# Optimization experiments

Measured on AMD Instinct MI355X. Metric: run time of the kernel, lower is better.

Reference implementation:

```python
import jax, jax.numpy as jnp
import numpy as np

N_STEPS = 20      # max(n_steps_al, n_steps_kc)
ALPHA   = 0.9     # membrane decay exp(-dt/tau_m)
V_TH    = 1.0     # spiking threshold
G_SOMA  = 0.3     # dendrite->axon coupling conductance (2-compartment KC)
APL_GAIN = 1.0    # graded APL gain
I_SCALE = 0.5     # graded ORN drive scale
BETA    = 10.0    # surrogate-gradient sharpness ('soft' sigmoid)

@jax.custom_vjp
def spike(x):
    return (x > 0).astype(x.dtype)

def _spike_fwd(x):
    return spike(x), x

def _spike_bwd(x, g):
    s = jax.nn.sigmoid(BETA * x)
    return (g * BETA * s * (1.0 - s),)

spike.defvjp(_spike_fwd, _spike_bwd)


def _sparse_w(key, shape, density):
    k1, k2 = jax.random.split(key)
    mask = jax.random.bernoulli(k1, density, shape)
    w = jax.random.uniform(k2, shape)
    return (mask * w).astype(jnp.float32)


def setup_inputs() -> dict:
    key = jax.random.key(0)
    ks = jax.random.split(key, 10)
    batch, n_or, n_orn, n_ln, n_pn, n_kc, n_odors = 4096, 21, 42, 56, 42, 2000, 34
    or_input = jax.random.uniform(ks[0], (batch, n_or), dtype=jnp.float32)
    or_gains = jnp.ones((n_or,), jnp.float32)
    # fixed OR->ORN mapping: OR i drives left (2i) and right (2i+1) ORNs
    m = np.zeros((n_or, n_orn), np.float32)
    for i in range(n_or):
        m[i, 2 * i] = 1.0
        m[i, 2 * i + 1] = 1.0
    mapping = jnp.asarray(m)
    orn_to_pn = _sparse_w(ks[1], (n_orn, n_pn), 0.3)
    orn_to_ln = _sparse_w(ks[2], (n_orn, n_ln), 0.3)
    ln_to_pn = _sparse_w(ks[3], (n_ln, n_pn), 0.3)
    pn_to_kc = _sparse_w(ks[4], (n_pn, n_kc), 0.15)  # ~6 PN claws per KC
    kc_to_apl = jax.random.uniform(ks[5], (n_kc, 1), dtype=jnp.float32) * 0.01
    apl_to_kc = jax.random.uniform(ks[6], (1, n_kc), dtype=jnp.float32)
    dec_w = jax.random.normal(ks[7], (n_kc, n_odors), dtype=jnp.float32) * 0.02
    dec_b = jnp.zeros((n_odors,), jnp.float32)
    return {"or_input": or_input, "or_gains": or_gains, "mapping": mapping,
            "orn_to_pn": orn_to_pn, "orn_to_ln": orn_to_ln, "ln_to_pn": ln_to_pn,
            "pn_to_kc": pn_to_kc, "kc_to_apl": kc_to_apl, "apl_to_kc": apl_to_kc,
            "dec_w": dec_w, "dec_b": dec_b}


def reference(or_input, or_gains, mapping, orn_to_pn, orn_to_ln, ln_to_pn,
              pn_to_kc, kc_to_apl, apl_to_kc, dec_w, dec_b):
    B = or_input.shape[0]
    n_orn, n_pn = orn_to_pn.shape
    n_ln = orn_to_ln.shape[1]
    n_kc = pn_to_kc.shape[1]
    # OR transduction: graded, learnable per-OR gain
    orn_drive = (or_input * jax.nn.softplus(or_gains)) @ mapping  # [B, n_orn]

    z = lambda n: jnp.zeros((B, n), or_input.dtype)
    carry0 = (z(n_orn), z(n_ln), z(n_pn), z(n_kc), z(n_kc), z(1), z(n_kc))

    def step(carry, _):
        v_orn, v_ln, v_pn, v_d, v_a, apl, kc_cnt = carry
        # ORN LIF driven by graded OR current
        v_orn = ALPHA * v_orn + I_SCALE * orn_drive
        s_orn = spike(v_orn - V_TH)
        v_orn = v_orn * (1.0 - s_orn)
        # LN LIF (lateral inhibition interneurons)
        v_ln = ALPHA * v_ln + s_orn @ orn_to_ln
        s_ln = spike(v_ln - V_TH)
        v_ln = v_ln * (1.0 - s_ln)
        # PN LIF: ORN excitation, LN inhibition
        v_pn = ALPHA * v_pn + s_orn @ orn_to_pn - s_ln @ ln_to_pn
        s_pn = spike(v_pn - V_TH)
        v_pn = v_pn * (1.0 - s_pn)
        # KC 2-compartment: dendrite gets PN input and APL inhibition
        v_d = ALPHA * v_d + s_pn @ pn_to_kc - apl @ apl_to_kc
        v_a = ALPHA * v_a + G_SOMA * (v_d - v_a)
        s_kc = spike(v_a - V_TH)
        v_a = v_a * (1.0 - s_kc)
        # APL: graded (non-spiking) global inhibition from KC spikes
        apl = APL_GAIN * jax.nn.relu(s_kc @ kc_to_apl)
        return (v_orn, v_ln, v_pn, v_d, v_a, apl, kc_cnt + s_kc), None

    carry, _ = jax.lax.scan(step, carry0, None, length=N_STEPS)
    kc_count = carry[-1]
    kc_rates = kc_count / N_STEPS
    logits = kc_rates @ dec_w + dec_b  # [B, n_odors]
    return logits
```

## Files before the change

kernel.cpp:

```cpp
#include <hip/hip_runtime.h>

#define NSTEPS 20
#define ALPHA  0.9f
#define VTH    1.0f
#define GSOMA  0.3f
#define ISCALE 0.5f

#define NOR  21
#define NORN 42
#define NLN  56
#define NPN  42
#define NKC  2000
#define NOD  34

#define TPB  256
#define KPER 8

__global__ __launch_bounds__(TPB)
void phase1_seq(const float* __restrict__ or_input,
                const float* __restrict__ or_gains,
                const float* __restrict__ mapping,
                const float* __restrict__ orn_to_pn,
                const float* __restrict__ orn_to_ln,
                const float* __restrict__ ln_to_pn,
                unsigned long long* __restrict__ gPN,
                int batch)
{
    __shared__ ulonglong2 sAB[4][NSTEPS];

    const int tid  = threadIdx.x;
    const int lane = tid & 63;
    const int wid  = tid >> 6;
    const int row  = blockIdx.x * 4 + wid;
    if (row >= batch) return;

    const int jl = lane < NLN ? lane : 0;
    float wOl[NORN];
#pragma unroll
    for (int o = 0; o < NORN; ++o) wOl[o] = orn_to_ln[o * NLN + jl];

    float spg = 0.f;
    if (lane < NOR) spg = log1pf(expf(or_gains[lane]));

    float drive = 0.f;
    {
        const float* x = or_input + (long)row * NOR;
        const int jo = lane < NORN ? lane : 0;
#pragma unroll
        for (int i = 0; i < NOR; ++i) {
            float g = __shfl(spg, i);
            drive += x[i] * g * mapping[i * NORN + jo];
        }
        drive *= ISCALE;
    }

    float v_orn = 0.f, v_ln = 0.f;
    for (int t = 0; t < NSTEPS; ++t) {
        bool so = false;
        if (lane < NORN) {
            v_orn = ALPHA * v_orn + drive;
            so = (v_orn - VTH) > 0.f;
            if (so) v_orn = 0.f;
        }
        const unsigned long long mOrn = __ballot(so);
        const unsigned int mo_lo = (unsigned int)mOrn;
        const unsigned int mo_hi = (unsigned int)(mOrn >> 32);

        float aln = 0.f;
#pragma unroll
        for (int o = 0; o < 32; ++o) aln += (float)((mo_lo >> o) & 1u) * wOl[o];
#pragma unroll
        for (int o = 32; o < NORN; ++o) aln += (float)((mo_hi >> (o - 32)) & 1u) * wOl[o];

        bool sl = false;
        if (lane < NLN) {
            v_ln = ALPHA * v_ln + aln;
            sl = (v_ln - VTH) > 0.f;
            if (sl) v_ln = 0.f;
        }
        const unsigned long long mLn = __ballot(sl);
        if (lane == 0) sAB[wid][t] = make_ulonglong2(mOrn, mLn);
    }
    asm volatile("" ::: "memory");

    const int jp = lane < NPN ? lane : 0;
    float wOp[NORN];
#pragma unroll
    for (int o = 0; o < NORN; ++o) wOp[o] = orn_to_pn[o * NPN + jp];

    float apn[NSTEPS];
#pragma unroll
    for (int t = 0; t < NSTEPS; ++t) {
        const unsigned long long mo = sAB[wid][t].x;
        const unsigned int lo = (unsigned int)mo;
        const unsigned int hi = (unsigned int)(mo >> 32);
        float a = 0.f;
#pragma unroll
        for (int o = 0; o < 32; ++o) a += (float)((lo >> o) & 1u) * wOp[o];
#pragma unroll
        for (int o = 32; o < NORN; ++o) a += (float)((hi >> (o - 32)) & 1u) * wOp[o];
        apn[t] = a;
    }
    asm volatile("" ::: "memory");

    float wLp[NLN];
#pragma unroll
    for (int l = 0; l < NLN; ++l) wLp[l] = ln_to_pn[l * NPN + jp];

    unsigned long long* outm = gPN + (long)row * NSTEPS;
    float v_pn = 0.f;
#pragma unroll
    for (int t = 0; t < NSTEPS; ++t) {
        const unsigned long long ml = sAB[wid][t].y;
        const unsigned int lo = (unsigned int)ml;
        const unsigned int hi = (unsigned int)(ml >> 32);
        float h = 0.f;
#pragma unroll
        for (int l = 0; l < 32; ++l) h += (float)((lo >> l) & 1u) * wLp[l];
#pragma unroll
        for (int l = 32; l < NLN; ++l) h += (float)((hi >> (l - 32)) & 1u) * wLp[l];

        bool sp = false;
        if (lane < NPN) {
            v_pn = ALPHA * v_pn + apn[t] - h;
            sp = (v_pn - VTH) > 0.f;
            if (sp) v_pn = 0.f;
        }
        const unsigned long long mPn = __ballot(sp);
        if (lane == 0) outm[t] = mPn;
    }
}

__global__ __launch_bounds__(TPB)
void phase2_kernel(const unsigned long long* __restrict__ g_masks,
                   const float* __restrict__ pn_to_kc,
                   const float* __restrict__ kc_to_apl,
                   const float* __restrict__ apl_to_kc,
                   const float* __restrict__ dec_w,
                   const float* __restrict__ dec_b,
                   float* __restrict__ out)
{
    __shared__ float sRed[2][4];
    __shared__ float sRed2[4 * NOD];

    const int tid  = threadIdx.x;
    const int lane = tid & 63;
    const int wid  = tid >> 6;
    const int b    = blockIdx.x;

    const int  kbase = tid * KPER;
    const bool act   = (kbase < NKC);
    float vd[KPER], va[KPER], cnt[KPER], wa2k[KPER], wk2a[KPER];
#pragma unroll
    for (int j = 0; j < KPER; ++j) { vd[j] = 0.f; va[j] = 0.f; cnt[j] = 0.f; }
    {
        const float4* a4 = (const float4*)(apl_to_kc + (act ? kbase : 0));
        const float4* k4 = (const float4*)(kc_to_apl + (act ? kbase : 0));
        float4 a0 = a4[0], a1 = a4[1], k0 = k4[0], k1 = k4[1];
        const float g = act ? 1.f : 0.f;
        wa2k[0] = g * a0.x; wa2k[1] = g * a0.y; wa2k[2] = g * a0.z; wa2k[3] = g * a0.w;
        wa2k[4] = g * a1.x; wa2k[5] = g * a1.y; wa2k[6] = g * a1.z; wa2k[7] = g * a1.w;
        wk2a[0] = g * k0.x; wk2a[1] = g * k0.y; wk2a[2] = g * k0.z; wk2a[3] = g * k0.w;
        wk2a[4] = g * k1.x; wk2a[5] = g * k1.y; wk2a[6] = g * k1.z; wk2a[7] = g * k1.w;
    }
    if (tid < 8) sRed[tid >> 2][tid & 3] = 0.f;
    __syncthreads();

    const unsigned long long* gm = g_masks + (long)b * NSTEPS;

    for (int t = 0; t < NSTEPS; ++t) {
        const float* rp = sRed[(t + 1) & 1];
        const float apl = fmaxf(rp[0] + rp[1] + rp[2] + rp[3], 0.f);

#pragma unroll
        for (int j = 0; j < KPER; ++j) vd[j] = ALPHA * vd[j] - apl * wa2k[j];

        unsigned long long m = gm[t];
        while (m) {
            const int p0 = __builtin_ctzll(m); m &= m - 1;
            int p1 = p0; float f1 = 0.f;
            if (m) { p1 = __builtin_ctzll(m); m &= m - 1; f1 = 1.f; }
            if (act) {
                const float4* w0 = (const float4*)(pn_to_kc + (long)p0 * NKC + kbase);
                const float4* w1 = (const float4*)(pn_to_kc + (long)p1 * NKC + kbase);
                float4 a0 = w0[0], a1 = w0[1];
                float4 b0 = w1[0], b1 = w1[1];
                vd[0] += a0.x; vd[1] += a0.y; vd[2] += a0.z; vd[3] += a0.w;
                vd[4] += a1.x; vd[5] += a1.y; vd[6] += a1.z; vd[7] += a1.w;
                vd[0] += f1 * b0.x; vd[1] += f1 * b0.y; vd[2] += f1 * b0.z; vd[3] += f1 * b0.w;
                vd[4] += f1 * b1.x; vd[5] += f1 * b1.y; vd[6] += f1 * b1.z; vd[7] += f1 * b1.w;
            }
        }

        float aplp = 0.f;
#pragma unroll
        for (int j = 0; j < KPER; ++j) {
            va[j] = ALPHA * va[j] + GSOMA * (vd[j] - va[j]);
            float s = (va[j] - VTH) > 0.f ? 1.f : 0.f;
            va[j] *= (1.f - s);
            cnt[j] += s;
            aplp += s * wk2a[j];
        }
        for (int off = 32; off > 0; off >>= 1) aplp += __shfl_xor(aplp, off, 64);
        if (lane == 0) sRed[t & 1][wid] = aplp;
        __syncthreads();
    }

    float acc[NOD];
#pragma unroll
    for (int o = 0; o < NOD; ++o) acc[o] = 0.f;
    if (act) {
#pragma unroll
        for (int j = 0; j < KPER; ++j) {
            float r = cnt[j] / 20.0f;
            if (r != 0.f) {
                const float* wr = dec_w + (long)(kbase + j) * NOD;
#pragma unroll
                for (int o = 0; o < NOD; ++o) acc[o] += r * wr[o];
            }
        }
    }
#pragma unroll
    for (int o = 0; o < NOD; ++o) {
        float v = acc[o];
        for (int off = 32; off > 0; off >>= 1) v += __shfl_xor(v, off, 64);
        if (lane == 0) sRed2[wid * NOD + o] = v;
    }
    __syncthreads();
    if (tid < NOD) {
        float v = sRed2[tid] + sRed2[NOD + tid] + sRed2[2 * NOD + tid] +
                  sRed2[3 * NOD + tid] + dec_b[tid];
        out[(long)b * NOD + tid] = v;
    }
}

__global__ __launch_bounds__(TPB)
void snn_fused(const float* __restrict__ or_input, const float* __restrict__ or_gains,
               const float* __restrict__ mapping, const float* __restrict__ orn_to_pn,
               const float* __restrict__ orn_to_ln, const float* __restrict__ ln_to_pn,
               const float* __restrict__ pn_to_kc, const float* __restrict__ kc_to_apl,
               const float* __restrict__ apl_to_kc, const float* __restrict__ dec_w,
               const float* __restrict__ dec_b, float* __restrict__ out)
{
    __shared__ float sW_ol[NORN * NLN];
    __shared__ float sW_op[NORN * NPN];
    __shared__ float sW_lp[NLN * NPN];
    __shared__ float sDrive[NORN];
    __shared__ float sSpg[NOR];
    __shared__ float sOrn[NORN];
    __shared__ float sLn[NLN];
    __shared__ float sApl;
    __shared__ float sRed[4];
    __shared__ float sRed2[4 * NOD];
    __shared__ unsigned long long sMask;

    const int tid = threadIdx.x;
    const int b   = blockIdx.x;

    for (int i = tid; i < NORN * NLN; i += TPB) sW_ol[i] = orn_to_ln[i];
    for (int i = tid; i < NORN * NPN; i += TPB) sW_op[i] = orn_to_pn[i];
    for (int i = tid; i < NLN * NPN;  i += TPB) sW_lp[i] = ln_to_pn[i];
    if (tid < NOR) sSpg[tid] = log1pf(expf(or_gains[tid]));
    if (tid == 0)  sApl = 0.f;
    __syncthreads();

    if (tid < NORN) {
        const float* x = or_input + (long)b * NOR;
        float d = 0.f;
        for (int i = 0; i < NOR; ++i) d += x[i] * sSpg[i] * mapping[i * NORN + tid];
        sDrive[tid] = d * ISCALE;
    }

    const int  kbase = tid * KPER;
    const bool act   = (kbase < NKC);
    float vd[KPER], va[KPER], cnt[KPER], wa2k[KPER], wk2a[KPER];
#pragma unroll
    for (int j = 0; j < KPER; ++j) {
        vd[j] = 0.f; va[j] = 0.f; cnt[j] = 0.f;
        wa2k[j] = act ? apl_to_kc[kbase + j] : 0.f;
        wk2a[j] = act ? kc_to_apl[kbase + j] : 0.f;
    }
    float v_orn = 0.f, v_ln = 0.f, v_pn = 0.f, v_pn_exc = 0.f;
    __syncthreads();

    for (int t = 0; t < NSTEPS; ++t) {
        if (tid < NORN) {
            v_orn = ALPHA * v_orn + sDrive[tid];
            float s = (v_orn - VTH) > 0.f ? 1.f : 0.f;
            v_orn *= (1.f - s);
            sOrn[tid] = s;
        }
        __syncthreads();
        if (tid < NLN) {
            float a = 0.f;
            for (int o = 0; o < NORN; ++o) a += sOrn[o] * sW_ol[o * NLN + tid];
            v_ln = ALPHA * v_ln + a;
            float s = (v_ln - VTH) > 0.f ? 1.f : 0.f;
            v_ln *= (1.f - s);
            sLn[tid] = s;
        } else if (tid >= 64 && tid < 64 + NPN) {
            const int j = tid - 64;
            float a = 0.f;
            for (int o = 0; o < NORN; ++o) a += sOrn[o] * sW_op[o * NPN + j];
            v_pn_exc = a;
        }
        __syncthreads();
        if (tid >= 64 && tid < 64 + NPN) {
            const int j = tid - 64;
            float inh = 0.f;
            for (int l = 0; l < NLN; ++l) inh += sLn[l] * sW_lp[l * NPN + j];
            v_pn = ALPHA * v_pn + v_pn_exc - inh;
            bool s = (v_pn - VTH) > 0.f;
            if (s) v_pn = 0.f;
            unsigned long long bal = __ballot(s);
            if (tid == 64) sMask = bal;
        }
        __syncthreads();
        {
            const float apl = sApl;
#pragma unroll
            for (int j = 0; j < KPER; ++j) vd[j] = ALPHA * vd[j] - apl * wa2k[j];
            unsigned long long m = sMask;
            while (m) {
                const int p = __builtin_ctzll(m);
                m &= m - 1;
                if (act) {
                    const float4* w = (const float4*)(pn_to_kc + (long)p * NKC + kbase);
                    float4 w0 = w[0], w1 = w[1];
                    vd[0] += w0.x; vd[1] += w0.y; vd[2] += w0.z; vd[3] += w0.w;
                    vd[4] += w1.x; vd[5] += w1.y; vd[6] += w1.z; vd[7] += w1.w;
                }
            }
            float aplp = 0.f;
#pragma unroll
            for (int j = 0; j < KPER; ++j) {
                va[j] = ALPHA * va[j] + GSOMA * (vd[j] - va[j]);
                float s = (va[j] - VTH) > 0.f ? 1.f : 0.f;
                va[j] *= (1.f - s);
                cnt[j] += s;
                aplp += s * wk2a[j];
            }
            for (int off = 32; off > 0; off >>= 1) aplp += __shfl_xor(aplp, off, 64);
            if ((tid & 63) == 0) sRed[tid >> 6] = aplp;
        }
        __syncthreads();
        if (tid == 0) {
            float a = sRed[0] + sRed[1] + sRed[2] + sRed[3];
            sApl = fmaxf(a, 0.f);
        }
    }

    float acc[NOD];
#pragma unroll
    for (int o = 0; o < NOD; ++o) acc[o] = 0.f;
    if (act) {
#pragma unroll
        for (int j = 0; j < KPER; ++j) {
            float r = cnt[j] / 20.0f;
            if (r != 0.f) {
                const float* wr = dec_w + (long)(kbase + j) * NOD;
#pragma unroll
                for (int o = 0; o < NOD; ++o) acc[o] += r * wr[o];
            }
        }
    }
#pragma unroll
    for (int o = 0; o < NOD; ++o) {
        float v = acc[o];
        for (int off = 32; off > 0; off >>= 1) v += __shfl_xor(v, off, 64);
        if ((tid & 63) == 0) sRed2[(tid >> 6) * NOD + o] = v;
    }
    __syncthreads();
    if (tid < NOD) {
        float v = sRed2[tid] + sRed2[NOD + tid] + sRed2[2 * NOD + tid] +
                  sRed2[3 * NOD + tid] + dec_b[tid];
        out[(long)b * NOD + tid] = v;
    }
}

extern "C" void kernel_launch(void* const* d_in, const int* in_sizes, int n_in,
                              void* d_out, int out_size, void* d_ws, size_t ws_size,
                              hipStream_t stream) {
    (void)n_in; (void)out_size;
    const float* or_input  = (const float*)d_in[0];
    const float* or_gains  = (const float*)d_in[1];
    const float* mapping   = (const float*)d_in[2];
    const float* orn_to_pn = (const float*)d_in[3];
    const float* orn_to_ln = (const float*)d_in[4];
    const float* ln_to_pn  = (const float*)d_in[5];
    const float* pn_to_kc  = (const float*)d_in[6];
    const float* kc_to_apl = (const float*)d_in[7];
    const float* apl_to_kc = (const float*)d_in[8];
    const float* dec_w     = (const float*)d_in[9];
    const float* dec_b     = (const float*)d_in[10];
    float* out = (float*)d_out;

    const int batch = in_sizes[0] / NOR;
    const size_t needPN = (size_t)batch * NSTEPS * sizeof(unsigned long long);

    if (ws_size >= needPN) {
        unsigned long long* gPN = (unsigned long long*)d_ws;
        hipLaunchKernelGGL(phase1_seq, dim3((batch + 3) / 4), dim3(TPB), 0, stream,
                           or_input, or_gains, mapping, orn_to_pn, orn_to_ln, ln_to_pn,
                           gPN, batch);
        hipLaunchKernelGGL(phase2_kernel, dim3(batch), dim3(TPB), 0, stream,
                           gPN, pn_to_kc, kc_to_apl, apl_to_kc, dec_w, dec_b, out);
    } else {
        hipLaunchKernelGGL(snn_fused, dim3(batch), dim3(TPB), 0, stream,
                           or_input, or_gains, mapping, orn_to_pn, orn_to_ln,
                           ln_to_pn, pn_to_kc, kc_to_apl, apl_to_kc, dec_w, dec_b, out);
    }
}
```

Measured before the change: 213.2 us.

## Split phase-1 into separate ORN/LN and PN kernels with 64-thread blocks

Splits the sequential phase-1 kernel into two launches. The first runs the ORN/LN dynamics and writes the ORN and LN spike masks to global workspace. The second loads both weight sets and computes PN dynamics, prefetching the next step's masks. The aim is lower register pressure per kernel and one wave per block for better scheduling, at the cost of an extra launch and a global round-trip for the masks. This also needs more workspace and falls back to the fused path if the workspace is too small.

```diff
diff --git a/kernel.cpp b/kernel.cpp
--- a/kernel.cpp
+++ b/kernel.cpp
@@ -16,22 +16,16 @@
 #define TPB  256
 #define KPER 8
 
-__global__ __launch_bounds__(TPB)
-void phase1_seq(const float* __restrict__ or_input,
-                const float* __restrict__ or_gains,
-                const float* __restrict__ mapping,
-                const float* __restrict__ orn_to_pn,
-                const float* __restrict__ orn_to_ln,
-                const float* __restrict__ ln_to_pn,
-                unsigned long long* __restrict__ gPN,
-                int batch)
+__global__ __launch_bounds__(64)
+void phase1a(const float* __restrict__ or_input,
+             const float* __restrict__ or_gains,
+             const float* __restrict__ mapping,
+             const float* __restrict__ orn_to_ln,
+             ulonglong2* __restrict__ gAB,
+             int batch)
 {
-    __shared__ ulonglong2 sAB[4][NSTEPS];
-
-    const int tid  = threadIdx.x;
-    const int lane = tid & 63;
-    const int wid  = tid >> 6;
-    const int row  = blockIdx.x * 4 + wid;
+    const int lane = threadIdx.x;
+    const int row  = blockIdx.x;
     if (row >= batch) return;
 
     const int jl = lane < NLN ? lane : 0;
@@ -55,6 +49,8 @@
     }
 
     float v_orn = 0.f, v_ln = 0.f;
+    ulonglong2* outm = gAB + (long)row * NSTEPS;
+
     for (int t = 0; t < NSTEPS; ++t) {
         bool so = false;
         if (lane < NORN) {
@@ -79,55 +75,64 @@
             if (sl) v_ln = 0.f;
         }
         const unsigned long long mLn = __ballot(sl);
-        if (lane == 0) sAB[wid][t] = make_ulonglong2(mOrn, mLn);
-    }
-    asm volatile("" ::: "memory");
+        if (lane == 0) outm[t] = make_ulonglong2(mOrn, mLn);
+    }
+}
+
+__global__ __launch_bounds__(64)
+void phase1b(const float* __restrict__ orn_to_pn,
+             const float* __restrict__ ln_to_pn,
+             const ulonglong2* __restrict__ gAB,
+             unsigned long long* __restrict__ gPN,
+             int batch)
+{
+    const int lane = threadIdx.x;
+    const int row  = blockIdx.x;
+    if (row >= batch) return;
 
     const int jp = lane < NPN ? lane : 0;
-    float wOp[NORN];
+    float wOp[NORN], wLp[NLN];
 #pragma unroll
     for (int o = 0; o < NORN; ++o) wOp[o] = orn_to_pn[o * NPN + jp];
-
-    float apn[NSTEPS];
-#pragma unroll
+#pragma unroll
+    for (int l = 0; l < NLN; ++l) wLp[l] = ln_to_pn[l * NPN + jp];
+
+    const ulonglong2* inm = gAB + (long)row * NSTEPS;
+    unsigned long long* outm = gPN + (long)row * NSTEPS;
+
+    float v_pn = 0.f;
+    ulonglong2 ab = inm[0];
+
     for (int t = 0; t < NSTEPS; ++t) {
-        const unsigned long long mo = sAB[wid][t].x;
-        const unsigned int lo = (unsigned int)mo;
-        const unsigned int hi = (unsigned int)(mo >> 32);
-        float a = 0.f;
-#pragma unroll
-        for (int o = 0; o < 32; ++o) a += (float)((lo >> o) & 1u) * wOp[o];
-#pragma unroll
-        for (int o = 32; o < NORN; ++o) a += (float)((hi >> (o - 32)) & 1u) * wOp[o];
-        apn[t] = a;
-    }
-    asm volatile("" ::: "memory");
-
-    float wLp[NLN];
-#pragma unroll
-    for (int l = 0; l < NLN; ++l) wLp[l] = ln_to_pn[l * NPN + jp];
-
-    unsigned long long* outm = gPN + (long)row * NSTEPS;
-    float v_pn = 0.f;
-#pragma unroll
-    for (int t = 0; t < NSTEPS; ++t) {
-        const unsigned long long ml = sAB[wid][t].y;
-        const unsigned int lo = (unsigned int)ml;
-        const unsigned int hi = (unsigned int)(ml >> 32);
+        ulonglong2 abn;
+        if (t < NSTEPS - 1) abn = inm[t + 1];
+
+        const unsigned int mo_lo = (unsigned int)ab.x;
+        const unsigned int mo_hi = (unsigned int)(ab.x >> 32);
+        const unsigned int ml_lo = (unsigned int)ab.y;
+        const unsigned int ml_hi = (unsigned int)(ab.y >> 32);
+
+        float apn = 0.f;
+#pragma unroll
+        for (int o = 0; o < 32; ++o) apn += (float)((mo_lo >> o) & 1u) * wOp[o];
+#pragma unroll
+        for (int o = 32; o < NORN; ++o) apn += (float)((mo_hi >> (o - 32)) & 1u) * wOp[o];
+
         float h = 0.f;
 #pragma unroll
-        for (int l = 0; l < 32; ++l) h += (float)((lo >> l) & 1u) * wLp[l];
-#pragma unroll
-        for (int l = 32; l < NLN; ++l) h += (float)((hi >> (l - 32)) & 1u) * wLp[l];
+        for (int l = 0; l < 32; ++l) h += (float)((ml_lo >> l) & 1u) * wLp[l];
+#pragma unroll
+        for (int l = 32; l < NLN; ++l) h += (float)((ml_hi >> (l - 32)) & 1u) * wLp[l];
 
         bool sp = false;
         if (lane < NPN) {
-            v_pn = ALPHA * v_pn + apn[t] - h;
+            v_pn = ALPHA * v_pn + apn - h;
             sp = (v_pn - VTH) > 0.f;
             if (sp) v_pn = 0.f;
         }
         const unsigned long long mPn = __ballot(sp);
         if (lane == 0) outm[t] = mPn;
+        ab = abn;
     }
 }
 
@@ -396,13 +401,16 @@
     float* out = (float*)d_out;
 
     const int batch = in_sizes[0] / NOR;
+    const size_t needAB = (size_t)batch * NSTEPS * sizeof(ulonglong2);
     const size_t needPN = (size_t)batch * NSTEPS * sizeof(unsigned long long);
 
-    if (ws_size >= needPN) {
-        unsigned long long* gPN = (unsigned long long*)d_ws;
-        hipLaunchKernelGGL(phase1_seq, dim3((batch + 3) / 4), dim3(TPB), 0, stream,
-                           or_input, or_gains, mapping, orn_to_pn, orn_to_ln, ln_to_pn,
-                           gPN, batch);
+    if (ws_size >= needAB + needPN) {
+        ulonglong2* gAB = (ulonglong2*)d_ws;
+        unsigned long long* gPN = (unsigned long long*)((char*)d_ws + needAB);
+        hipLaunchKernelGGL(phase1a, dim3(batch), dim3(64), 0, stream,
+                           or_input, or_gains, mapping, orn_to_ln, gAB, batch);
+        hipLaunchKernelGGL(phase1b, dim3(batch), dim3(64), 0, stream,
+                           orn_to_pn, ln_to_pn, gAB, gPN, batch);
         hipLaunchKernelGGL(phase2_kernel, dim3(batch), dim3(TPB), 0, stream,
                            gPN, pn_to_kc, kc_to_apl, apl_to_kc, dec_w, dec_b, out);
     } else {
```

After: 209.4 us. No clear change (-1.8%).
